# Performance work log

Hardware: AMD Instinct MI355X
Metric: run time of the kernel (lower is better)

## Reference

```python
import jax, jax.numpy as jnp
import numpy as np

B, C, H = 64, 64, 32

def _pm_cross_pairs(ks):
    # Replicates PM_cross(2, ks): pairs (i, i+j) ordered by gap j=1..ks-1, then i.
    a, b = [], []
    for j in range(1, ks):
        for i in range(ks - j):
            a.append(i)
            b.append(i + j)
    return np.array(a, dtype=np.int32), np.array(b, dtype=np.int32)

def setup_inputs() -> dict:
    key = jax.random.key(0)
    k1, k2 = jax.random.split(key)
    ia, ib = _pm_cross_pairs(H)           # 496 pairs for H=32
    hk = ia.shape[0] + 2 * H              # 560
    x = jax.random.normal(k1, (B, C, H, H), dtype=jnp.float32)
    weight = 0.1 * jax.random.normal(k2, (C, H, hk, H), dtype=jnp.float32)
    return {"x": x, "weight": weight, "idx_a": jnp.asarray(ia), "idx_b": jnp.asarray(ib)}

def reference(x, weight, idx_a, idx_b):
    # cross-term products along last axis: [B,C,H,P]
    cross = x[..., idx_a] * x[..., idx_b]
    feat = jnp.concatenate([x, x * x, cross], axis=-1)  # [B,C,H,Hk]
    # per-(channel,row) grouped matmul
    return jnp.einsum('bcij,cijo->bcio', feat, weight)
```

## Files before the change

### kernel.cpp

```cpp
#include <hip/hip_runtime.h>

#define NB 64
#define NC 64
#define NH 32
#define HK 560
#define NOCT 96
#define XSTR 57

typedef __bf16 bf16x8 __attribute__((ext_vector_type(8)));
typedef float f32x4 __attribute__((ext_vector_type(4)));

__global__ __launch_bounds__(256, 4) void hconv_kernel(
    const float* __restrict__ x, const float* __restrict__ w,
    const int* __restrict__ idx_a, const int* __restrict__ idx_b,
    float* __restrict__ out)
{
    __shared__ __align__(16) float smem[4 * 64 * 33];
    float* s_x = smem;
    unsigned* s_desc = (unsigned*)&smem[NB * XSTR];
    float* s_stage = &smem[NB * XSTR + NOCT];

    const int t = threadIdx.x;
    const int g = blockIdx.x;
    const int c = g >> 5, i = g & 31;

    {
        const int xrow = t >> 2, seg = t & 3;
        const float* xr = x + (((size_t)xrow * NC + c) * NH + i) * NH + seg * 8;
        float4 v0 = *(const float4*)(xr);
        float4 v1 = *(const float4*)(xr + 4);
        float* dst = &s_x[xrow * XSTR + 8 + seg * 8];
        dst[0] = v0.x; dst[1] = v0.y; dst[2] = v0.z; dst[3] = v0.w;
        dst[4] = v1.x; dst[5] = v1.y; dst[6] = v1.z; dst[7] = v1.w;
        if (seg == 0) {
            float* r0 = &s_x[xrow * XSTR];
            #pragma unroll
            for (int m = 0; m < 8; ++m) {
                r0[m] = 0.0f;
                r0[40 + m] = 0.0f;
                r0[48 + m] = 1.0f;
            }
        }
    }

    if (t < NOCT) {
        unsigned pa, pb, ko;
        const int mm = t % 24, ws = t / 24;
        const int q = mm * 4 + ws;
        if (mm >= 21)   { pa = 0u; pb = 0u; ko = 0u; }
        else if (q < 4) { pa = 8u + 8u * q; pb = 48u; ko = 8u * q; }
        else if (q < 8) { unsigned u = q - 4; pa = pb = 8u + 8u * u; ko = 32u + 8u * u; }
        else {
            unsigned qq = q - 8, j, a;
            if (qq < 28)      { j = 1 + qq / 4;         a = qq % 4; }
            else if (qq < 52) { j = 8 + (qq - 28) / 3;  a = (qq - 28) % 3; }
            else if (qq < 68) { j = 16 + (qq - 52) / 2; a = (qq - 52) % 2; }
            else              { j = 24 + (qq - 68);     a = 0; }
            ko = 64u + (j - 1) * 32u - (j * (j - 1)) / 2u + 8u * a;
            pa = 8u + 8u * a; pb = pa + j;
            if (ko > 552u) { unsigned sh = ko - 552u; ko = 552u; pa -= sh; pb -= sh; }
        }
        s_desc[t] = pa | (pb << 6) | (ko << 12);
    }

    const int wv = t >> 6, lane = t & 63;
    const int lr = lane & 15, lq = lane >> 4;
    const float* wbase = w + (size_t)(c * NH + i) * HK * NH;

    __syncthreads();

    unsigned d6[6];
    #pragma unroll
    for (int k = 0; k < 6; ++k)
        d6[k] = s_desc[(3 * wv + (k >> 1)) * 8 + (k & 1) * 4 + lq];

    f32x4 acc[4][2];
    #pragma unroll
    for (int r = 0; r < 4; ++r) {
        acc[r][0] = (f32x4){0.f, 0.f, 0.f, 0.f};
        acc[r][1] = (f32x4){0.f, 0.f, 0.f, 0.f};
    }

    f32x4 gA[4], gB[4];

#define GLOAD(G, K) { \
    _Pragma("unroll") \
    for (int o_ = 0; o_ < 4; ++o_) { \
        unsigned dd_ = (unsigned)__builtin_amdgcn_readlane((int)d6[K], 16 * o_); \
        const float* wp_ = wbase + (size_t)(dd_ >> 12) * NH + 4 * lane; \
        G[o_] = *(const f32x4*)wp_; } }

#define SWRITE(G) { \
    float* tb_ = s_stage + wv * 1056 + (lane >> 3) * 33 + (lane & 7) * 4; \
    _Pragma("unroll") \
    for (int o_ = 0; o_ < 4; ++o_) \
        _Pragma("unroll") \
        for (int w_ = 0; w_ < 4; ++w_) \
            tb_[o_ * 264 + w_] = G[o_][w_]; }

#define STEP(K, DOLD, GLD, DOWR, GWR) { \
    bf16x8 b0_, b1_; \
    { const float* rb_ = s_stage + wv * 1056 + lq * 264 + lr; \
      _Pragma("unroll") \
      for (int j_ = 0; j_ < 8; ++j_) { \
          b0_[j_] = (__bf16)rb_[j_ * 33]; \
          b1_[j_] = (__bf16)rb_[j_ * 33 + 16]; } } \
    if (DOLD) GLOAD(GLD, (K) + 2); \
    if (DOWR) SWRITE(GWR); \
    const unsigned d_ = d6[K]; \
    _Pragma("unroll") \
    for (int rt_ = 0; rt_ < 4; ++rt_) { \
        const float* xr_ = &s_x[(rt_ * 16 + lr) * XSTR]; \
        const float* qa_ = xr_ + (d_ & 63u); \
        const float* qb_ = xr_ + ((d_ >> 6) & 63u); \
        bf16x8 a_; \
        _Pragma("unroll") \
        for (int j_ = 0; j_ < 8; ++j_) a_[j_] = (__bf16)(qa_[j_] * qb_[j_]); \
        acc[rt_][0] = __builtin_amdgcn_mfma_f32_16x16x32_bf16(a_, b0_, acc[rt_][0], 0, 0, 0); \
        acc[rt_][1] = __builtin_amdgcn_mfma_f32_16x16x32_bf16(a_, b1_, acc[rt_][1], 0, 0, 0); } }

    GLOAD(gA, 0);
    GLOAD(gB, 1);
    SWRITE(gA);
    STEP(0, 1, gA, 1, gB);
    STEP(1, 1, gB, 1, gA);
    STEP(2, 1, gA, 1, gB);
    STEP(3, 1, gB, 1, gA);
    STEP(4, 0, gA, 1, gB);
    STEP(5, 0, gA, 0, gA);

#undef STEP
#undef SWRITE
#undef GLOAD

    __syncthreads();

    #pragma unroll
    for (int rt = 0; rt < 4; ++rt)
        #pragma unroll
        for (int nh = 0; nh < 2; ++nh)
            #pragma unroll
            for (int r = 0; r < 4; ++r)
                smem[(wv * NB + rt * 16 + lq * 4 + r) * 33 + nh * 16 + lr] =
                    acc[rt][nh][r];

    __syncthreads();

    {
        const int b = t >> 2, m0 = (t & 3) * 8;
        float s0[8];
        #pragma unroll
        for (int m = 0; m < 8; ++m) s0[m] = smem[b * 33 + m0 + m];
        #pragma unroll
        for (int wv2 = 1; wv2 < 4; ++wv2)
            #pragma unroll
            for (int m = 0; m < 8; ++m)
                s0[m] += smem[(wv2 * NB + b) * 33 + m0 + m];
        float* op = out + (((size_t)b * NC + c) * NH + i) * NH + m0;
        float4 o0 = {s0[0], s0[1], s0[2], s0[3]};
        float4 o1 = {s0[4], s0[5], s0[6], s0[7]};
        *(float4*)op = o0;
        *(float4*)(op + 4) = o1;
    }
}

extern "C" void kernel_launch(void* const* d_in, const int* in_sizes, int n_in,
                              void* d_out, int out_size, void* d_ws, size_t ws_size,
                              hipStream_t stream) {
    const float* x = (const float*)d_in[0];
    const float* w = (const float*)d_in[1];
    const int* idx_a = (const int*)d_in[2];
    const int* idx_b = (const int*)d_in[3];
    float* out = (float*)d_out;
    hconv_kernel<<<dim3(NC * NH), dim3(256), 0, stream>>>(x, w, idx_a, idx_b, out);
}
```

Before: 233.0 us.

## Compute pair descriptors in registers and reuse x windows via sliding registers

Work descriptors are now computed per lane in registers instead of being built in shared memory, which removes a syncthreads and the descriptor table. Chunks are reassigned so that each lane keeps a fixed first operand (qx) in registers and slides the second operand window (wx) by one element per step, loading only one new value instead of eight. The first weight global loads are issued before the x tile is staged, so they overlap. This costs more registers, so the occupancy hint drops from 4 to 3 blocks per SM, and it adds inactive padding slots that skip loads.

```diff
diff --git a/kernel.cpp b/kernel.cpp
--- a/kernel.cpp
+++ b/kernel.cpp
@@ -4,31 +4,78 @@
 #define NC 64
 #define NH 32
 #define HK 560
-#define NOCT 96
 #define XSTR 57
 
 typedef __bf16 bf16x8 __attribute__((ext_vector_type(8)));
 typedef float f32x4 __attribute__((ext_vector_type(4)));
 
-__global__ __launch_bounds__(256, 4) void hconv_kernel(
+__global__ __launch_bounds__(256, 3) void hconv_kernel(
     const float* __restrict__ x, const float* __restrict__ w,
     const int* __restrict__ idx_a, const int* __restrict__ idx_b,
     float* __restrict__ out)
 {
     __shared__ __align__(16) float smem[4 * 64 * 33];
     float* s_x = smem;
-    unsigned* s_desc = (unsigned*)&smem[NB * XSTR];
-    float* s_stage = &smem[NB * XSTR + NOCT];
+    float* s_stage = &smem[NB * XSTR];
 
     const int t = threadIdx.x;
     const int g = blockIdx.x;
     const int c = g >> 5, i = g & 31;
 
+    const int wv = t >> 6, lane = t & 63;
+    const int lr = lane & 15, lq = lane >> 4;
+    const float* wbase = w + (size_t)(c * NH + i) * HK * NH;
+    const int xrow = t >> 2, seg = t & 3;
+    const float* xr = x + (((size_t)xrow * NC + c) * NH + i) * NH + seg * 8;
+
+    float4 v0 = *(const float4*)(xr);
+    float4 v1 = *(const float4*)(xr + 4);
+
+    const int c2 = lq * 4 + wv;
+    int a, cc;
+    if (c2 < 6)       { a = 0; cc = c2; }
+    else if (c2 < 11) { a = 1; cc = c2 - 6; }
+    else if (c2 < 14) { a = 2; cc = c2 - 11; }
+    else              { a = 3; cc = c2 - 14; }
+    const int cnt = (a == 0) ? 33 : (a == 1) ? 25 : (a == 2) ? 17 : 9;
+    const unsigned pa0 = 8u + 8u * (unsigned)a;
+
+    unsigned d6[6];
+    #pragma unroll
+    for (int p = 0; p < 6; ++p) {
+        const int m = cc * 6 + p;
+        unsigned pa = pa0, pb, ko, act;
+        if (m >= cnt)    { act = 3u; pb = pa0; ko = 1023u; }
+        else if (m == 0) { act = 1u; pb = pa0; ko = 32u + 8u * a; }
+        else if (m == 5) { act = 1u; pb = 48u; ko = 8u * a; }
+        else {
+            const int j = (m < 5) ? m : m - 1;
+            ko = 64u + (unsigned)((j - 1) * 32 - (j * (j - 1)) / 2) + 8u * a;
+            pb = pa0 + (unsigned)j;
+            if (ko > 552u) { unsigned s = ko - 552u; ko = 552u; pa = pa0 - s; pb -= s; act = 2u; }
+            else act = (p == 0) ? 1u : 0u;
+        }
+        d6[p] = pa | (pb << 6) | (ko << 12) | (act << 22);
+    }
+
+    f32x4 gA[4], gB[4];
+
+#define GLOAD(G, K) { \
+    _Pragma("unroll") \
+    for (int o_ = 0; o_ < 4; ++o_) { \
+        unsigned dd_ = (unsigned)__builtin_amdgcn_readlane((int)d6[K], 16 * o_); \
+        unsigned ko_ = (dd_ >> 12) & 1023u; \
+        if (ko_ != 1023u) { \
+            const float* wp_ = wbase + (size_t)ko_ * NH + 4 * lane; \
+            G[o_] = *(const f32x4*)wp_; \
+        } else { \
+            G[o_] = (f32x4){0.f, 0.f, 0.f, 0.f}; \
+        } } }
+
+    GLOAD(gA, 0);
+    GLOAD(gB, 1);
+
     {
-        const int xrow = t >> 2, seg = t & 3;
-        const float* xr = x + (((size_t)xrow * NC + c) * NH + i) * NH + seg * 8;
-        float4 v0 = *(const float4*)(xr);
-        float4 v1 = *(const float4*)(xr + 4);
         float* dst = &s_x[xrow * XSTR + 8 + seg * 8];
         dst[0] = v0.x; dst[1] = v0.y; dst[2] = v0.z; dst[3] = v0.w;
         dst[4] = v1.x; dst[5] = v1.y; dst[6] = v1.z; dst[7] = v1.w;
@@ -43,52 +90,12 @@
         }
     }
 
-    if (t < NOCT) {
-        unsigned pa, pb, ko;
-        const int mm = t % 24, ws = t / 24;
-        const int q = mm * 4 + ws;
-        if (mm >= 21)   { pa = 0u; pb = 0u; ko = 0u; }
-        else if (q < 4) { pa = 8u + 8u * q; pb = 48u; ko = 8u * q; }
-        else if (q < 8) { unsigned u = q - 4; pa = pb = 8u + 8u * u; ko = 32u + 8u * u; }
-        else {
-            unsigned qq = q - 8, j, a;
-            if (qq < 28)      { j = 1 + qq / 4;         a = qq % 4; }
-            else if (qq < 52) { j = 8 + (qq - 28) / 3;  a = (qq - 28) % 3; }
-            else if (qq < 68) { j = 16 + (qq - 52) / 2; a = (qq - 52) % 2; }
-            else              { j = 24 + (qq - 68);     a = 0; }
-            ko = 64u + (j - 1) * 32u - (j * (j - 1)) / 2u + 8u * a;
-            pa = 8u + 8u * a; pb = pa + j;
-            if (ko > 552u) { unsigned sh = ko - 552u; ko = 552u; pa -= sh; pb -= sh; }
-        }
-        s_desc[t] = pa | (pb << 6) | (ko << 12);
-    }
-
-    const int wv = t >> 6, lane = t & 63;
-    const int lr = lane & 15, lq = lane >> 4;
-    const float* wbase = w + (size_t)(c * NH + i) * HK * NH;
-
-    __syncthreads();
-
-    unsigned d6[6];
-    #pragma unroll
-    for (int k = 0; k < 6; ++k)
-        d6[k] = s_desc[(3 * wv + (k >> 1)) * 8 + (k & 1) * 4 + lq];
-
     f32x4 acc[4][2];
     #pragma unroll
     for (int r = 0; r < 4; ++r) {
         acc[r][0] = (f32x4){0.f, 0.f, 0.f, 0.f};
         acc[r][1] = (f32x4){0.f, 0.f, 0.f, 0.f};
     }
-
-    f32x4 gA[4], gB[4];
-
-#define GLOAD(G, K) { \
-    _Pragma("unroll") \
-    for (int o_ = 0; o_ < 4; ++o_) { \
-        unsigned dd_ = (unsigned)__builtin_amdgcn_readlane((int)d6[K], 16 * o_); \
-        const float* wp_ = wbase + (size_t)(dd_ >> 12) * NH + 4 * lane; \
-        G[o_] = *(const f32x4*)wp_; } }
 
 #define SWRITE(G) { \
     float* tb_ = s_stage + wv * 1056 + (lane >> 3) * 33 + (lane & 7) * 4; \
@@ -97,6 +104,17 @@
         _Pragma("unroll") \
         for (int w_ = 0; w_ < 4; ++w_) \
             tb_[o_ * 264 + w_] = G[o_][w_]; }
+
+    __syncthreads();
+
+    float qx[4][8];
+    #pragma unroll
+    for (int rt = 0; rt < 4; ++rt)
+        #pragma unroll
+        for (int m = 0; m < 8; ++m)
+            qx[rt][m] = s_x[(rt * 16 + lr) * XSTR + (int)pa0 + m];
+
+    float wx[4][8];
 
 #define STEP(K, DOLD, GLD, DOWR, GWR) { \
     bf16x8 b0_, b1_; \
@@ -105,22 +123,39 @@
       for (int j_ = 0; j_ < 8; ++j_) { \
           b0_[j_] = (__bf16)rb_[j_ * 33]; \
           b1_[j_] = (__bf16)rb_[j_ * 33 + 16]; } } \
-    if (DOLD) GLOAD(GLD, (K) + 2); \
+    if (DOLD) GLOAD(GLD, (((K) + 2) % 6)); \
     if (DOWR) SWRITE(GWR); \
     const unsigned d_ = d6[K]; \
+    const unsigned act_ = d_ >> 22; \
+    const int paf_ = (int)(d_ & 63u), pbf_ = (int)((d_ >> 6) & 63u); \
+    if (act_ == 0u) {                       \
+        _Pragma("unroll") \
+        for (int rt_ = 0; rt_ < 4; ++rt_) { \
+            _Pragma("unroll") \
+            for (int m_ = 0; m_ < 7; ++m_) wx[rt_][m_] = wx[rt_][m_ + 1]; \
+            wx[rt_][7] = s_x[(rt_ * 16 + lr) * XSTR + pbf_ + 7]; } \
+    } else if (act_ <= 2u) {                \
+        if (act_ == 2u) { \
+            _Pragma("unroll") \
+            for (int rt_ = 0; rt_ < 4; ++rt_) \
+                _Pragma("unroll") \
+                for (int m_ = 0; m_ < 8; ++m_) \
+                    qx[rt_][m_] = s_x[(rt_ * 16 + lr) * XSTR + paf_ + m_]; } \
+        _Pragma("unroll") \
+        for (int rt_ = 0; rt_ < 4; ++rt_) \
+            _Pragma("unroll") \
+            for (int m_ = 0; m_ < 8; ++m_) \
+                wx[rt_][m_] = s_x[(rt_ * 16 + lr) * XSTR + pbf_ + m_]; \
+    }                                       \
     _Pragma("unroll") \
     for (int rt_ = 0; rt_ < 4; ++rt_) { \
-        const float* xr_ = &s_x[(rt_ * 16 + lr) * XSTR]; \
-        const float* qa_ = xr_ + (d_ & 63u); \
-        const float* qb_ = xr_ + ((d_ >> 6) & 63u); \
         bf16x8 a_; \
         _Pragma("unroll") \
-        for (int j_ = 0; j_ < 8; ++j_) a_[j_] = (__bf16)(qa_[j_] * qb_[j_]); \
+        for (int j_ = 0; j_ < 8; ++j_) \
+            a_[j_] = (__bf16)(qx[rt_][j_] * wx[rt_][j_]); \
         acc[rt_][0] = __builtin_amdgcn_mfma_f32_16x16x32_bf16(a_, b0_, acc[rt_][0], 0, 0, 0); \
         acc[rt_][1] = __builtin_amdgcn_mfma_f32_16x16x32_bf16(a_, b1_, acc[rt_][1], 0, 0, 0); } }
 
-    GLOAD(gA, 0);
-    GLOAD(gB, 1);
     SWRITE(gA);
     STEP(0, 1, gA, 1, gB);
     STEP(1, 1, gB, 1, gA);
```

Measured after the change: 321.6 us. +38.0%, slower.
